# Kernel optimization log

Hardware: AMD Instinct MI355X
Metric: run time of the kernel (lower is better)

The kernel has to match this reference:

```python
import jax, jax.numpy as jnp
import numpy as np

D_MODEL = 1024
N_HEADS = 16
D_HEAD = D_MODEL // N_HEADS
B, T = 2, 2048


def setup_inputs() -> dict:
    key = jax.random.key(0)
    k1, k2, k3 = jax.random.split(key, 3)
    x = jax.random.normal(k1, (B, T, D_MODEL), dtype=jnp.float32)
    # torch nn.Linear weights: y = x @ W.T, W has shape [out, in]
    W_qkv = jax.random.normal(k2, (3 * D_MODEL, D_MODEL), dtype=jnp.float32) * (1.0 / np.sqrt(D_MODEL))
    W_out = jax.random.normal(k3, (D_MODEL, D_MODEL), dtype=jnp.float32) * (1.0 / np.sqrt(D_MODEL))
    return {"x": x, "W_qkv": W_qkv, "W_out": W_out}


def reference(x, W_qkv, W_out):
    Bb, Tt, Dd = x.shape
    qkv = (x @ W_qkv.T).reshape(Bb, Tt, 3, N_HEADS, D_HEAD)
    q, k, v = qkv[:, :, 0], qkv[:, :, 1], qkv[:, :, 2]  # [B,T,H,d]
    q = q.transpose(0, 2, 1, 3)  # [B,H,T,d]
    k = k.transpose(0, 2, 1, 3)
    v = v.transpose(0, 2, 1, 3)
    scale = 1.0 / np.sqrt(D_HEAD)
    scores = jnp.einsum('bhqd,bhkd->bhqk', q, k) * scale  # [B,H,T,T]
    causal = jnp.tril(jnp.ones((Tt, Tt), dtype=bool))
    scores = jnp.where(causal, scores, -jnp.inf)
    A = jax.nn.softmax(scores, axis=-1)
    AV = jnp.einsum('bhqk,bhkd->bhqd', A, v)
    AAV = jnp.einsum('bhqk,bhkd->bhqd', A, AV)  # twicing correction
    out = 2.0 * AV - AAV  # [B,H,T,d]
    out = out.transpose(0, 2, 1, 3).reshape(Bb, Tt, Dd)
    return out @ W_out.T
```

## Files before the change

### kernel.cpp

```cpp
#include <hip/hip_runtime.h>
#include <hip/hip_bf16.h>

#define T_SEQ  2048
#define DMODEL 1024
#define NH     16
#define DH     64
#define NTOK   4096
#define QSCALE 0.18033688011112042f
#define M_FIX  16.0f

typedef unsigned short u16;
typedef short s16x8 __attribute__((ext_vector_type(8)));
typedef unsigned short u16x8 __attribute__((ext_vector_type(8)));
typedef float f32x4 __attribute__((ext_vector_type(4)));

__device__ __forceinline__ u16 f2bf(float f) {
  unsigned u = __float_as_uint(f);
  u += 0x7FFFu + ((u >> 16) & 1u);
  return (u16)(u >> 16);
}
__device__ __forceinline__ unsigned pk2(float a, float b) {
  __hip_bfloat162 h = __float22bfloat162_rn(make_float2(a, b));
  unsigned u;
  __builtin_memcpy(&u, &h, 4);
  return u;
}
__device__ __forceinline__ unsigned pk2z(float a, float b) {
  return __builtin_amdgcn_perm(__float_as_uint(b), __float_as_uint(a), 0x07060302);
}
__device__ __forceinline__ float bf2f(u16 x) {
  return __uint_as_float(((unsigned)x) << 16);
}
__device__ __forceinline__ void async_cp16(const u16* g, u16* l) {
  __builtin_amdgcn_global_load_lds(
      (const __attribute__((address_space(1))) unsigned*)g,
      (__attribute__((address_space(3))) unsigned*)l, 16, 0, 0);
}

__global__ void cast_to_bf16(const float* __restrict__ in, u16* __restrict__ out, int n4) {
  int i = blockIdx.x * blockDim.x + threadIdx.x;
  if (i >= n4) return;
  float4 v = reinterpret_cast<const float4*>(in)[i];
  ushort4 r;
  r.x = f2bf(v.x); r.y = f2bf(v.y); r.z = f2bf(v.z); r.w = f2bf(v.w);
  reinterpret_cast<ushort4*>(out)[i] = r;
}

__global__ __launch_bounds__(256) void gemm_qkv(
    const u16* __restrict__ A, const u16* __restrict__ Bm,
    u16* __restrict__ outQ, u16* __restrict__ outK, u16* __restrict__ outV) {
  __shared__ __align__(16) u16 SM[24576];
  const int tid = threadIdx.x, wave = tid >> 6, lane = tid & 63;
  const int f15 = lane & 15, quad = lane >> 4;
  const int bm = blockIdx.x * 128, bn = blockIdx.y * 128;
  const int wr = wave >> 1, wc = wave & 1;
  const int K = DMODEL;

  f32x4 acc[4][4] = {};

  const u16* Ag0 = A  + (size_t)(bm + (2 * wave) * 16 + f15) * K + quad * 8;
  const u16* Ag1 = A  + (size_t)(bm + (2 * wave + 1) * 16 + f15) * K + quad * 8;
  const u16* Bg0 = Bm + (size_t)(bn + (2 * wave) * 16 + f15) * K + quad * 8;
  const u16* Bg1 = Bm + (size_t)(bn + (2 * wave + 1) * 16 + f15) * K + quad * 8;
  u16* LA0 = SM + (2 * wave) * 512 + lane * 8;
  u16* LA1 = SM + (2 * wave + 1) * 512 + lane * 8;
  u16* LB0 = SM + 4096 + (2 * wave) * 512 + lane * 8;
  u16* LB1 = SM + 4096 + (2 * wave + 1) * 512 + lane * 8;

  const int KT = K >> 5;
  async_cp16(Ag0, LA0); async_cp16(Ag1, LA1);
  async_cp16(Bg0, LB0); async_cp16(Bg1, LB1);
  async_cp16(Ag0 + 32, LA0 + 8192); async_cp16(Ag1 + 32, LA1 + 8192);
  async_cp16(Bg0 + 32, LB0 + 8192); async_cp16(Bg1 + 32, LB1 + 8192);

  int bufr = 0, bufw = 2;
  for (int kt = 0; kt < KT; kt++) {
    if (kt + 1 < KT) asm volatile("s_waitcnt vmcnt(4)" ::: "memory");
    else             asm volatile("s_waitcnt vmcnt(0)" ::: "memory");
    __builtin_amdgcn_s_barrier();
    __builtin_amdgcn_sched_barrier(0);
    if (kt + 2 < KT) {
      const int k0 = (kt + 2) * 32;
      const int o = bufw * 8192;
      async_cp16(Ag0 + k0, LA0 + o); async_cp16(Ag1 + k0, LA1 + o);
      async_cp16(Bg0 + k0, LB0 + o); async_cp16(Bg1 + k0, LB1 + o);
    }
    const u16* Af = SM + bufr * 8192;
    const u16* Bf = Af + 4096;
    s16x8 af[4], bfr[4];
#pragma unroll
    for (int mi = 0; mi < 4; mi++)
      af[mi] = *reinterpret_cast<const s16x8*>(Af + (wr * 4 + mi) * 512 + lane * 8);
#pragma unroll
    for (int ni = 0; ni < 4; ni++)
      bfr[ni] = *reinterpret_cast<const s16x8*>(Bf + (wc * 4 + ni) * 512 + lane * 8);
#pragma unroll
    for (int mi = 0; mi < 4; mi++)
#pragma unroll
      for (int ni = 0; ni < 4; ni++)
        acc[mi][ni] = __builtin_amdgcn_mfma_f32_16x16x32_bf16(af[mi], bfr[ni], acc[mi][ni], 0, 0, 0);
    bufr = (bufr == 2) ? 0 : bufr + 1;
    bufw = (bufw == 2) ? 0 : bufw + 1;
  }

  u16* Cs = SM;
  if (bn < 2048) {
    const float scale = (bn < 1024) ? QSCALE : 1.0f;
#pragma unroll
    for (int h2 = 0; h2 < 2; h2++) {
      __syncthreads();
      if (wr == h2) {
#pragma unroll
        for (int mi = 0; mi < 4; mi++)
#pragma unroll
          for (int ni = 0; ni < 4; ni++) {
            int c = wc * 64 + ni * 16 + f15;
#pragma unroll
            for (int r = 0; r < 4; r++)
              Cs[(mi * 16 + quad * 4 + r) * 136 + c] = f2bf(acc[mi][ni][r] * scale);
          }
      }
      __syncthreads();
      const int row = tid >> 2, cs = (tid & 3) * 32;
      const int gm = bm + h2 * 64 + row;
#pragma unroll
      for (int c8 = 0; c8 < 4; c8++) {
        int gc = bn + cs + c8 * 8;
        u16x8 v = *reinterpret_cast<const u16x8*>(&Cs[row * 136 + cs + c8 * 8]);
        int which = gc >> 10, hh = (gc >> 6) & 15, d = gc & 63;
        u16* dst = (which ? outK : outQ) + ((size_t)hh * NTOK + gm) * 64 + d;
        *reinterpret_cast<u16x8*>(dst) = v;
      }
    }
  } else {
    const int bnV = bn - 2048;
#pragma unroll
    for (int h2 = 0; h2 < 2; h2++) {
      __syncthreads();
      if (wr == h2) {
#pragma unroll
        for (int mi = 0; mi < 4; mi++)
#pragma unroll
          for (int ni = 0; ni < 4; ni++) {
            int c = wc * 64 + ni * 16 + f15;
#pragma unroll
            for (int r = 0; r < 4; r++)
              Cs[(mi * 16 + quad * 4 + r) * 138 + c] = f2bf(acc[mi][ni][r]);
          }
      }
      __syncthreads();
      const int fd = tid >> 3, s8 = (tid & 7) * 8;
      const int tb = ((s8 >> 5) & 1) * 32 + ((s8 >> 3) & 3) * 4;
      const int gmb = bm + h2 * 64;
#pragma unroll
      for (int p = 0; p < 4; p++) {
        const int d = p * 32 + fd;
        u16x8 vv;
#pragma unroll
        for (int j = 0; j < 4; j++) vv[j] = Cs[(tb + j) * 138 + d];
#pragma unroll
        for (int j = 0; j < 4; j++) vv[4 + j] = Cs[(tb + 16 + j) * 138 + d];
        *reinterpret_cast<u16x8*>(outV + (size_t)(bnV + d) * NTOK + gmb + s8) = vv;
      }
    }
  }
}

__global__ __launch_bounds__(256) void gemm_out(
    const u16* __restrict__ A, const u16* __restrict__ Bm, float* __restrict__ outF) {
  __shared__ __align__(16) u16 SM[18432];
  const int tid = threadIdx.x, wave = tid >> 6, lane = tid & 63;
  const int f15 = lane & 15, quad = lane >> 4;
  const int bm = blockIdx.x * 64, bn = blockIdx.y * 128;
  const int wr = wave >> 1, wc = wave & 1;
  const int K = DMODEL, N = DMODEL;

  f32x4 acc[2][4] = {};

  const u16* Ag = A  + (size_t)(bm + wave * 16 + f15) * K + quad * 8;
  const u16* Bg0 = Bm + (size_t)(bn + (2 * wave) * 16 + f15) * K + quad * 8;
  const u16* Bg1 = Bm + (size_t)(bn + (2 * wave + 1) * 16 + f15) * K + quad * 8;
  u16* LA  = SM + wave * 512 + lane * 8;
  u16* LB0 = SM + 2048 + (2 * wave) * 512 + lane * 8;
  u16* LB1 = SM + 2048 + (2 * wave + 1) * 512 + lane * 8;

  const int KT = K >> 5;
  async_cp16(Ag, LA); async_cp16(Bg0, LB0); async_cp16(Bg1, LB1);
  async_cp16(Ag + 32, LA + 6144); async_cp16(Bg0 + 32, LB0 + 6144); async_cp16(Bg1 + 32, LB1 + 6144);

  int bufr = 0, bufw = 2;
  for (int kt = 0; kt < KT; kt++) {
    if (kt + 1 < KT) asm volatile("s_waitcnt vmcnt(3)" ::: "memory");
    else             asm volatile("s_waitcnt vmcnt(0)" ::: "memory");
    __builtin_amdgcn_s_barrier();
    __builtin_amdgcn_sched_barrier(0);
    if (kt + 2 < KT) {
      const int k0 = (kt + 2) * 32;
      const int o = bufw * 6144;
      async_cp16(Ag + k0, LA + o); async_cp16(Bg0 + k0, LB0 + o); async_cp16(Bg1 + k0, LB1 + o);
    }
    const u16* Af = SM + bufr * 6144;
    const u16* Bf = Af + 2048;
    s16x8 af[2], bfr[4];
#pragma unroll
    for (int mi = 0; mi < 2; mi++)
      af[mi] = *reinterpret_cast<const s16x8*>(Af + (wr * 2 + mi) * 512 + lane * 8);
#pragma unroll
    for (int ni = 0; ni < 4; ni++)
      bfr[ni] = *reinterpret_cast<const s16x8*>(Bf + (wc * 4 + ni) * 512 + lane * 8);
#pragma unroll
    for (int mi = 0; mi < 2; mi++)
#pragma unroll
      for (int ni = 0; ni < 4; ni++)
        acc[mi][ni] = __builtin_amdgcn_mfma_f32_16x16x32_bf16(af[mi], bfr[ni], acc[mi][ni], 0, 0, 0);
    bufr = (bufr == 2) ? 0 : bufr + 1;
    bufw = (bufw == 2) ? 0 : bufw + 1;
  }

#pragma unroll
  for (int mi = 0; mi < 2; mi++)
#pragma unroll
    for (int ni = 0; ni < 4; ni++)
#pragma unroll
      for (int r = 0; r < 4; r++)
        outF[(size_t)(bm + wr * 32 + mi * 16 + quad * 4 + r) * N + bn + wc * 64 + ni * 16 + f15] =
            acc[mi][ni][r];
}

template <int PASS>
__global__ __launch_bounds__(256) void attn_pass(
    const u16* __restrict__ Qb, const u16* __restrict__ Kb, const u16* __restrict__ Vsrc,
    float* __restrict__ LinvG, u16* __restrict__ Vp2, u16* __restrict__ TW) {
  __shared__ __align__(16) u16 SM[16384];
  const int tid = threadIdx.x, wave = tid >> 6, lane = tid & 63;
  const int f15 = lane & 15, quad = lane >> 4;
  const int bid = blockIdx.x;
  const int y = (bid & 7) * 4 + ((bid >> 3) & 3);
  const int b = y >> 4, h = y & 15;
  const int g = bid >> 5, a = g & 7;
  const int gq = g >> 3;
  const int qt = (gq == 0) ? (31 - a) : (gq == 1) ? (8 + a) : (gq == 2) ? (23 - a) : a;
  const int q0 = qt * 64;
  const int ntiles = qt + 1;
  const size_t qk_base = ((size_t)h * NTOK + (size_t)b * T_SEQ) * 64;
  const size_t vt_base = (size_t)h * 64 * NTOK + (size_t)b * T_SEQ;

  const int qw = q0 + 16 * wave;
  s16x8 qf0, qf1;
  {
    const u16* qp = Qb + qk_base + (size_t)(qw + f15) * 64 + quad * 8;
    qf0 = *reinterpret_cast<const s16x8*>(qp);
    qf1 = *reinterpret_cast<const s16x8*>(qp + 32);
  }
  float invl_r = 0.f;
  if (PASS == 1) invl_r = LinvG[(size_t)y * T_SEQ + qw + f15];

  f32x4 accO[4] = {};
  float l_acc = 0.f;

  const u16* Kg = Kb  + qk_base + (size_t)(wave * 16 + f15) * 64 + quad * 8;
  const u16* Vg = Vsrc + vt_base + (size_t)(wave * 16 + f15) * NTOK + quad * 8;
  u16* LK = SM + (wave * 2) * 512 + lane * 8;
  u16* LV = SM + 4096 + (wave * 2) * 512 + lane * 8;

  async_cp16(Kg, LK); async_cp16(Kg + 32, LK + 512);
  async_cp16(Vg, LV); async_cp16(Vg + 32, LV + 512);
  __syncthreads();

  for (int ti = 0; ti < ntiles; ti++) {
    const int buf = ti & 1;
    if (ti + 1 < ntiles) {
      const int j1 = (ti + 1) * 64;
      const int o = (buf ^ 1) * 8192;
      async_cp16(Kg + (size_t)j1 * 64, LK + o);
      async_cp16(Kg + (size_t)j1 * 64 + 32, LK + o + 512);
      async_cp16(Vg + j1, LV + o);
      async_cp16(Vg + j1 + 32, LV + o + 512);
    }
    const u16* Kf = SM + buf * 8192;
    const u16* Vf = SM + buf * 8192 + 4096;

    f32x4 accS[4] = {};
#pragma unroll
    for (int st = 0; st < 4; st++) {
      s16x8 k0 = *reinterpret_cast<const s16x8*>(Kf + (st * 2) * 512 + lane * 8);
      s16x8 k1 = *reinterpret_cast<const s16x8*>(Kf + (st * 2 + 1) * 512 + lane * 8);
      accS[st] = __builtin_amdgcn_mfma_f32_16x16x32_bf16(k0, qf0, accS[st], 0, 0, 0);
      accS[st] = __builtin_amdgcn_mfma_f32_16x16x32_bf16(k1, qf1, accS[st], 0, 0, 0);
    }
    union pbu { s16x8 v; unsigned u[4]; } pb0, pb1;
    if (ti < qt) {
#pragma unroll
      for (int st = 0; st < 4; st++) {
        float e0 = __builtin_amdgcn_exp2f(accS[st][0] - M_FIX);
        float e1 = __builtin_amdgcn_exp2f(accS[st][1] - M_FIX);
        float e2 = __builtin_amdgcn_exp2f(accS[st][2] - M_FIX);
        float e3 = __builtin_amdgcn_exp2f(accS[st][3] - M_FIX);
        if (PASS == 0) l_acc += (e0 + e1) + (e2 + e3);
        unsigned w0 = pk2z(e0, e1), w1 = pk2z(e2, e3);
        if (st < 2) { pb0.u[(st & 1) * 2] = w0; pb0.u[(st & 1) * 2 + 1] = w1; }
        else        { pb1.u[(st & 1) * 2] = w0; pb1.u[(st & 1) * 2 + 1] = w1; }
      }
    } else {
      const int qrel = 16 * wave + f15;
#pragma unroll
      for (int st = 0; st < 4; st++) {
        const int jb = st * 16 + quad * 4;
        float e0 = (jb + 0 <= qrel) ? __builtin_amdgcn_exp2f(accS[st][0] - M_FIX) : 0.f;
        float e1 = (jb + 1 <= qrel) ? __builtin_amdgcn_exp2f(accS[st][1] - M_FIX) : 0.f;
        float e2 = (jb + 2 <= qrel) ? __builtin_amdgcn_exp2f(accS[st][2] - M_FIX) : 0.f;
        float e3 = (jb + 3 <= qrel) ? __builtin_amdgcn_exp2f(accS[st][3] - M_FIX) : 0.f;
        if (PASS == 0) l_acc += (e0 + e1) + (e2 + e3);
        unsigned w0 = pk2z(e0, e1), w1 = pk2z(e2, e3);
        if (st < 2) { pb0.u[(st & 1) * 2] = w0; pb0.u[(st & 1) * 2 + 1] = w1; }
        else        { pb1.u[(st & 1) * 2] = w0; pb1.u[(st & 1) * 2 + 1] = w1; }
      }
    }
#pragma unroll
    for (int mt = 0; mt < 4; mt++) {
      s16x8 v0 = *reinterpret_cast<const s16x8*>(Vf + (mt * 2) * 512 + lane * 8);
      s16x8 v1 = *reinterpret_cast<const s16x8*>(Vf + (mt * 2 + 1) * 512 + lane * 8);
      accO[mt] = __builtin_amdgcn_mfma_f32_16x16x32_bf16(v0, pb0.v, accO[mt], 0, 0, 0);
      accO[mt] = __builtin_amdgcn_mfma_f32_16x16x32_bf16(v1, pb1.v, accO[mt], 0, 0, 0);
    }
    __syncthreads();
  }

  if (PASS == 0) {
    float l = l_acc;
    l += __shfl_xor(l, 16);
    l += __shfl_xor(l, 32);
    invl_r = 1.0f / l;
    if (quad == 0) LinvG[(size_t)y * T_SEQ + qw + f15] = invl_r;
  }

  if (PASS == 0) {
    u16* E = SM;
    const int ql = 16 * wave + f15;
    const int slot = (ql >> 5) * 32 + ((ql >> 2) & 3) * 8 + ((ql >> 4) & 1) * 4 + (ql & 3);
#pragma unroll
    for (int mt = 0; mt < 4; mt++)
#pragma unroll
      for (int r = 0; r < 4; r++)
        E[(mt * 16 + quad * 4 + r) * 68 + slot] = f2bf(accO[mt][r] * invl_r);
    __syncthreads();
    const int d = tid >> 2, s = (tid & 3) * 16;
    const u16* vg2 = Vsrc + vt_base + (size_t)d * NTOK + q0 + s;
    u16* og = Vp2 + vt_base + (size_t)d * NTOK + q0 + s;
#pragma unroll
    for (int g2 = 0; g2 < 2; g2++) {
      u16x8 vv = *reinterpret_cast<const u16x8*>(vg2 + g2 * 8);
      u16x8 ee = *reinterpret_cast<const u16x8*>(&E[d * 68 + s + g2 * 8]);
      u16x8 oo;
#pragma unroll
      for (int i = 0; i < 8; i++) oo[i] = f2bf(2.0f * bf2f(vv[i]) - bf2f(ee[i]));
      *reinterpret_cast<u16x8*>(og + g2 * 8) = oo;
    }
  } else {
    u16* E2 = SM;
#pragma unroll
    for (int mt = 0; mt < 4; mt++) {
      uint2 w;
      w.x = pk2(accO[mt][0] * invl_r, accO[mt][1] * invl_r);
      w.y = pk2(accO[mt][2] * invl_r, accO[mt][3] * invl_r);
      *reinterpret_cast<uint2*>(&E2[(16 * wave + f15) * 72 + mt * 16 + quad * 4]) = w;
    }
    __syncthreads();
    const int q = tid >> 2, s = (tid & 3) * 16;
    u16* dst = TW + ((size_t)b * T_SEQ + q0 + q) * DMODEL + h * 64 + s;
    *reinterpret_cast<u16x8*>(dst) = *reinterpret_cast<const u16x8*>(&E2[q * 72 + s]);
    *reinterpret_cast<u16x8*>(dst + 8) = *reinterpret_cast<const u16x8*>(&E2[q * 72 + s + 8]);
  }
}

extern "C" void kernel_launch(void* const* d_in, const int* in_sizes, int n_in,
                              void* d_out, int out_size, void* d_ws, size_t ws_size,
                              hipStream_t stream) {
  const float* x    = (const float*)d_in[0];
  const float* Wqkv = (const float*)d_in[1];
  const float* Wout = (const float*)d_in[2];
  float* out = (float*)d_out;
  char* ws = (char*)d_ws;

  u16*   Xb    = (u16*)(ws + 0);
  u16*   Wqkvb = (u16*)(ws + 8388608);
  u16*   Woutb = (u16*)(ws + 14680064);
  u16*   Qb    = (u16*)(ws + 16777216);
  u16*   Kb    = (u16*)(ws + 25165824);
  u16*   Vtp   = (u16*)(ws + 33554432);
  u16*   TW    = (u16*)(ws + 41943040);
  u16*   Vp2   = (u16*)(ws + 50331648);
  float* LinvG = (float*)(ws + 58720256);

  cast_to_bf16<<<4096, 256, 0, stream>>>(x, Xb, 1048576);
  cast_to_bf16<<<3072, 256, 0, stream>>>(Wqkv, Wqkvb, 786432);
  cast_to_bf16<<<1024, 256, 0, stream>>>(Wout, Woutb, 262144);

  gemm_qkv<<<dim3(32, 24), 256, 0, stream>>>(Xb, Wqkvb, Qb, Kb, Vtp);

  attn_pass<0><<<1024, 256, 0, stream>>>(Qb, Kb, Vtp, LinvG, Vp2, nullptr);
  attn_pass<1><<<1024, 256, 0, stream>>>(Qb, Kb, Vp2, LinvG, nullptr, TW);

  gemm_out<<<dim3(64, 8), 256, 0, stream>>>(TW, Woutb, out);
}
```

Before: 233.2 us.

## Enlarge QKV GEMM tile to 256x256 with 8 waves and 4-stage pipeline

The QKV projection GEMM now uses 256x256 output tiles computed by 512 threads (8 waves in a 2x4 grid, each owning 128x64), with a four-buffer async global-to-LDS pipeline that prefetches three k-steps ahead. MFMA issue is wrapped in s_setprio, and the epilogue is restaged in four 64-row chunks through a wider LDS buffer. The aim is more operand reuse per LDS load and deeper latency hiding. In exchange there are far fewer blocks (192 against 768), which may underfill the GPU's compute units, and LDS and register use per block rise substantially.

```diff
diff --git a/kernel.cpp b/kernel.cpp
--- a/kernel.cpp
+++ b/kernel.cpp
@@ -46,17 +46,17 @@
   reinterpret_cast<ushort4*>(out)[i] = r;
 }
 
-__global__ __launch_bounds__(256) void gemm_qkv(
+__global__ __launch_bounds__(512, 2) void gemm_qkv(
     const u16* __restrict__ A, const u16* __restrict__ Bm,
     u16* __restrict__ outQ, u16* __restrict__ outK, u16* __restrict__ outV) {
-  __shared__ __align__(16) u16 SM[24576];
+  __shared__ __align__(16) u16 SM[65536];
   const int tid = threadIdx.x, wave = tid >> 6, lane = tid & 63;
   const int f15 = lane & 15, quad = lane >> 4;
-  const int bm = blockIdx.x * 128, bn = blockIdx.y * 128;
-  const int wr = wave >> 1, wc = wave & 1;
+  const int bm = blockIdx.x * 256, bn = blockIdx.y * 256;
+  const int wm = wave >> 2, wn = wave & 3;
   const int K = DMODEL;
 
-  f32x4 acc[4][4] = {};
+  f32x4 acc[8][4] = {};
 
   const u16* Ag0 = A  + (size_t)(bm + (2 * wave) * 16 + f15) * K + quad * 8;
   const u16* Ag1 = A  + (size_t)(bm + (2 * wave + 1) * 16 + f15) * K + quad * 8;
@@ -64,70 +64,74 @@
   const u16* Bg1 = Bm + (size_t)(bn + (2 * wave + 1) * 16 + f15) * K + quad * 8;
   u16* LA0 = SM + (2 * wave) * 512 + lane * 8;
   u16* LA1 = SM + (2 * wave + 1) * 512 + lane * 8;
-  u16* LB0 = SM + 4096 + (2 * wave) * 512 + lane * 8;
-  u16* LB1 = SM + 4096 + (2 * wave + 1) * 512 + lane * 8;
-
-  const int KT = K >> 5;
-  async_cp16(Ag0, LA0); async_cp16(Ag1, LA1);
-  async_cp16(Bg0, LB0); async_cp16(Bg1, LB1);
-  async_cp16(Ag0 + 32, LA0 + 8192); async_cp16(Ag1 + 32, LA1 + 8192);
-  async_cp16(Bg0 + 32, LB0 + 8192); async_cp16(Bg1 + 32, LB1 + 8192);
-
-  int bufr = 0, bufw = 2;
-  for (int kt = 0; kt < KT; kt++) {
-    if (kt + 1 < KT) asm volatile("s_waitcnt vmcnt(4)" ::: "memory");
-    else             asm volatile("s_waitcnt vmcnt(0)" ::: "memory");
+  u16* LB0 = SM + 8192 + (2 * wave) * 512 + lane * 8;
+  u16* LB1 = SM + 8192 + (2 * wave + 1) * 512 + lane * 8;
+
+  const int S = K >> 5;
+#pragma unroll
+  for (int s = 0; s < 3; s++) {
+    const int k0 = s * 32, o = s * 16384;
+    async_cp16(Ag0 + k0, LA0 + o); async_cp16(Ag1 + k0, LA1 + o);
+    async_cp16(Bg0 + k0, LB0 + o); async_cp16(Bg1 + k0, LB1 + o);
+  }
+
+  for (int s = 0; s < S; s++) {
+    if (s < S - 2)       asm volatile("s_waitcnt vmcnt(8)" ::: "memory");
+    else if (s == S - 2) asm volatile("s_waitcnt vmcnt(4)" ::: "memory");
+    else                 asm volatile("s_waitcnt vmcnt(0)" ::: "memory");
     __builtin_amdgcn_s_barrier();
     __builtin_amdgcn_sched_barrier(0);
-    if (kt + 2 < KT) {
-      const int k0 = (kt + 2) * 32;
-      const int o = bufw * 8192;
+    if (s + 3 < S) {
+      const int k0 = (s + 3) * 32, o = ((s + 3) & 3) * 16384;
       async_cp16(Ag0 + k0, LA0 + o); async_cp16(Ag1 + k0, LA1 + o);
       async_cp16(Bg0 + k0, LB0 + o); async_cp16(Bg1 + k0, LB1 + o);
     }
-    const u16* Af = SM + bufr * 8192;
-    const u16* Bf = Af + 4096;
-    s16x8 af[4], bfr[4];
-#pragma unroll
-    for (int mi = 0; mi < 4; mi++)
-      af[mi] = *reinterpret_cast<const s16x8*>(Af + (wr * 4 + mi) * 512 + lane * 8);
+    const u16* Sl = SM + (s & 3) * 16384;
+    s16x8 af[8], bfr[4];
 #pragma unroll
     for (int ni = 0; ni < 4; ni++)
-      bfr[ni] = *reinterpret_cast<const s16x8*>(Bf + (wc * 4 + ni) * 512 + lane * 8);
-#pragma unroll
-    for (int mi = 0; mi < 4; mi++)
+      bfr[ni] = *reinterpret_cast<const s16x8*>(Sl + 8192 + (wn * 4 + ni) * 512 + lane * 8);
+#pragma unroll
+    for (int mi = 0; mi < 8; mi++)
+      af[mi] = *reinterpret_cast<const s16x8*>(Sl + (wm * 8 + mi) * 512 + lane * 8);
+    __builtin_amdgcn_s_setprio(1);
+#pragma unroll
+    for (int mi = 0; mi < 8; mi++)
 #pragma unroll
       for (int ni = 0; ni < 4; ni++)
         acc[mi][ni] = __builtin_amdgcn_mfma_f32_16x16x32_bf16(af[mi], bfr[ni], acc[mi][ni], 0, 0, 0);
-    bufr = (bufr == 2) ? 0 : bufr + 1;
-    bufw = (bufw == 2) ? 0 : bufw + 1;
-  }
-
+    __builtin_amdgcn_s_setprio(0);
+  }
+
+  __syncthreads();
   u16* Cs = SM;
+  const int ST = 264;
   if (bn < 2048) {
     const float scale = (bn < 1024) ? QSCALE : 1.0f;
 #pragma unroll
-    for (int h2 = 0; h2 < 2; h2++) {
+    for (int c = 0; c < 4; c++) {
+      if (c) __syncthreads();
+      if (wm == (c >> 1)) {
+#pragma unroll
+        for (int mi2 = 0; mi2 < 4; mi2++) {
+          const int mi = (c & 1) * 4 + mi2;
+#pragma unroll
+          for (int ni = 0; ni < 4; ni++) {
+            const int col = (wn * 4 + ni) * 16 + f15;
+#pragma unroll
+            for (int r = 0; r < 4; r++)
+              Cs[(mi2 * 16 + quad * 4 + r) * ST + col] = f2bf(acc[mi][ni][r] * scale);
+          }
+        }
+      }
       __syncthreads();
-      if (wr == h2) {
-#pragma unroll
-        for (int mi = 0; mi < 4; mi++)
-#pragma unroll
-          for (int ni = 0; ni < 4; ni++) {
-            int c = wc * 64 + ni * 16 + f15;
-#pragma unroll
-            for (int r = 0; r < 4; r++)
-              Cs[(mi * 16 + quad * 4 + r) * 136 + c] = f2bf(acc[mi][ni][r] * scale);
-          }
-      }
-      __syncthreads();
-      const int row = tid >> 2, cs = (tid & 3) * 32;
-      const int gm = bm + h2 * 64 + row;
+      const int row = tid >> 3, cb = (tid & 7) * 32;
+      const int gm = bm + c * 64 + row;
 #pragma unroll
       for (int c8 = 0; c8 < 4; c8++) {
-        int gc = bn + cs + c8 * 8;
-        u16x8 v = *reinterpret_cast<const u16x8*>(&Cs[row * 136 + cs + c8 * 8]);
-        int which = gc >> 10, hh = (gc >> 6) & 15, d = gc & 63;
+        const int gc = bn + cb + c8 * 8;
+        u16x8 v = *reinterpret_cast<const u16x8*>(&Cs[row * ST + cb + c8 * 8]);
+        const int which = gc >> 10, hh = (gc >> 6) & 15, d = gc & 63;
         u16* dst = (which ? outK : outQ) + ((size_t)hh * NTOK + gm) * 64 + d;
         *reinterpret_cast<u16x8*>(dst) = v;
       }
@@ -135,31 +139,33 @@
   } else {
     const int bnV = bn - 2048;
 #pragma unroll
-    for (int h2 = 0; h2 < 2; h2++) {
+    for (int c = 0; c < 4; c++) {
+      if (c) __syncthreads();
+      if (wm == (c >> 1)) {
+#pragma unroll
+        for (int mi2 = 0; mi2 < 4; mi2++) {
+          const int mi = (c & 1) * 4 + mi2;
+#pragma unroll
+          for (int ni = 0; ni < 4; ni++) {
+            const int col = (wn * 4 + ni) * 16 + f15;
+#pragma unroll
+            for (int r = 0; r < 4; r++)
+              Cs[(mi2 * 16 + quad * 4 + r) * ST + col] = f2bf(acc[mi][ni][r]);
+          }
+        }
+      }
       __syncthreads();
-      if (wr == h2) {
-#pragma unroll
-        for (int mi = 0; mi < 4; mi++)
-#pragma unroll
-          for (int ni = 0; ni < 4; ni++) {
-            int c = wc * 64 + ni * 16 + f15;
-#pragma unroll
-            for (int r = 0; r < 4; r++)
-              Cs[(mi * 16 + quad * 4 + r) * 138 + c] = f2bf(acc[mi][ni][r]);
-          }
-      }
-      __syncthreads();
-      const int fd = tid >> 3, s8 = (tid & 7) * 8;
+      const int fc = tid >> 3, s8 = (tid & 7) * 8;
       const int tb = ((s8 >> 5) & 1) * 32 + ((s8 >> 3) & 3) * 4;
-      const int gmb = bm + h2 * 64;
+      const int gmb = bm + c * 64;
 #pragma unroll
       for (int p = 0; p < 4; p++) {
-        const int d = p * 32 + fd;
+        const int d = p * 64 + fc;
         u16x8 vv;
 #pragma unroll
-        for (int j = 0; j < 4; j++) vv[j] = Cs[(tb + j) * 138 + d];
-#pragma unroll
-        for (int j = 0; j < 4; j++) vv[4 + j] = Cs[(tb + 16 + j) * 138 + d];
+        for (int j = 0; j < 4; j++) vv[j] = Cs[(tb + j) * ST + d];
+#pragma unroll
+        for (int j = 0; j < 4; j++) vv[4 + j] = Cs[(tb + 16 + j) * ST + d];
         *reinterpret_cast<u16x8*>(outV + (size_t)(bnV + d) * NTOK + gmb + s8) = vv;
       }
     }
@@ -396,7 +402,7 @@
   cast_to_bf16<<<3072, 256, 0, stream>>>(Wqkv, Wqkvb, 786432);
   cast_to_bf16<<<1024, 256, 0, stream>>>(Wout, Woutb, 262144);
 
-  gemm_qkv<<<dim3(32, 24), 256, 0, stream>>>(Xb, Wqkvb, Qb, Kb, Vtp);
+  gemm_qkv<<<dim3(16, 12), 512, 0, stream>>>(Xb, Wqkvb, Qb, Kb, Vtp);
 
   attn_pass<0><<<1024, 256, 0, stream>>>(Qb, Kb, Vtp, LinvG, Vp2, nullptr);
   attn_pass<1><<<1024, 256, 0, stream>>>(Qb, Kb, Vp2, LinvG, nullptr, TW);
```

New measurement: 222.7 us. 1.05x faster.
